# Performance work log

Measured on AMD Instinct MI355X. Metric: run time of the kernel, lower is better.

The kernel has to match this reference:

```python
import jax, jax.numpy as jnp
import numpy as np

B, S, D, H, N = 4, 2048, 512, 8, 64
HD = D // H  # head dim


def setup_inputs() -> dict:
    key = jax.random.key(0)
    ks = jax.random.split(key, 4)
    s = 0.02  # xavier-ish init scale
    return {
        "x": jax.random.normal(ks[0], (B, S, D), jnp.float32),
        "in_proj_w": jax.random.normal(ks[1], (3 * D, D), jnp.float32) * s,
        "in_proj_b": jnp.zeros((3 * D,), jnp.float32),
        "out_proj_w": jax.random.normal(ks[2], (D, D), jnp.float32) * s,
        "out_proj_b": jnp.zeros((D,), jnp.float32),
        "content_w": jax.random.normal(ks[3], (N, D), jnp.float32) * s,
        "content_b": jnp.zeros((N,), jnp.float32),
        "k_input": 16,
    }


def _fwd_core(x, in_proj_w, in_proj_b, out_proj_w, out_proj_b, content_w, content_b):
    # torch nn.MultiheadAttention (batch_first, eval/no dropout), self-attention
    qkv = jnp.einsum("bsd,ed->bse", x, in_proj_w) + in_proj_b  # [B,S,3D]
    q, k, v = jnp.split(qkv, 3, axis=-1)
    to_heads = lambda t: t.reshape(B, S, H, HD).transpose(0, 2, 1, 3)  # [B,H,S,hd]
    q, k, v = to_heads(q), to_heads(k), to_heads(v)
    scores = jnp.einsum("bhqd,bhkd->bhqk", q, k) / jnp.sqrt(jnp.float32(HD))
    attn = jax.nn.softmax(scores, axis=-1)  # [B,H,S,S] (need_weights=True path)
    ctx = jnp.einsum("bhqk,bhkd->bhqd", attn, v)
    ctx = ctx.transpose(0, 2, 1, 3).reshape(B, S, D)
    attended = jnp.einsum("bsd,ed->bse", ctx, out_proj_w) + out_proj_b  # [B,S,D]

    # content_to_neuron
    aff = jnp.einsum("bsd,nd->bsn", attended, content_w) + content_b  # [B,S,N]

    # position importance: mean over heads, sum over keys, normalize
    pos_imp = attn.mean(axis=1).sum(axis=2)  # [B,S]
    pos_imp = pos_imp / (pos_imp.sum(axis=1, keepdims=True) + 1e-8)

    weighted = (aff * pos_imp[..., None]).sum(axis=1)  # [B,N]
    final = 0.5 * weighted + 0.3 * aff.max(axis=1) + 0.2 * aff.mean(axis=1)
    probs = jax.nn.softmax(final, axis=-1)
    return final, probs, attended


def reference(x, in_proj_w, in_proj_b, out_proj_w, out_proj_b, content_w, content_b, k_input):
    final, probs, attended = _fwd_core(
        x, in_proj_w, in_proj_b, out_proj_w, out_proj_b, content_w, content_b
    )
    _, input_idx = jax.lax.top_k(final, k_input)  # [B,k]
    one_hot = jnp.zeros_like(probs).at[jnp.arange(B)[:, None], input_idx].set(1.0)
    # straight-through: value == one_hot, gradient flows through probs
    routing_weights = jax.lax.stop_gradient(one_hot - probs) + probs
    return input_idx, routing_weights, attended
```

## Files before the change

### kernel.cpp

```cpp
#include <hip/hip_runtime.h>
#include <hip/hip_bf16.h>

typedef unsigned short u16;
typedef __bf16 bf16x8 __attribute__((ext_vector_type(8)));
typedef u16 u16x8 __attribute__((ext_vector_type(8)));
typedef u16 u16x4 __attribute__((ext_vector_type(4)));
typedef float f32x4 __attribute__((ext_vector_type(4)));

__device__ __forceinline__ u16 f2bf(float f) {
  union { float f; unsigned u; } v; v.f = f;
  return (u16)((v.u + 0x7FFFu + ((v.u >> 16) & 1u)) >> 16);
}
__device__ __forceinline__ float bf2f(u16 h) {
  union { unsigned u; float f; } v; v.u = ((unsigned)h) << 16;
  return v.f;
}
struct BfPair { u16 hi, lo; };
__device__ __forceinline__ BfPair split2(float f) {
  BfPair r;
  r.hi = f2bf(f);
  r.lo = f2bf(f - bf2f(r.hi));
  return r;
}
__device__ __forceinline__ bf16x8 as_bf16x8(u16x8 u) {
  union { u16x8 u; bf16x8 b; } v; v.u = u; return v.b;
}

#define MFMA16(a, b, c) __builtin_amdgcn_mfma_f32_16x16x32_bf16((a), (b), (c), 0, 0, 0)

#define GLD16(gp, lp)                                                          \
  __builtin_amdgcn_global_load_lds(                                            \
      (const __attribute__((address_space(1))) void*)(gp),                     \
      (__attribute__((address_space(3))) void*)(lp), 16, 0, 0)

__global__ __launch_bounds__(256) void split_kernel(
    const float* __restrict__ src, u16* __restrict__ hi, u16* __restrict__ lo, int n4)
{
  int i = blockIdx.x * 256 + threadIdx.x;
  if (i >= n4) return;
  f32x4 v = ((const f32x4*)src)[i];
  u16x4 h, l;
  #pragma unroll
  for (int j = 0; j < 4; j++) { BfPair p = split2(v[j]); h[j] = p.hi; l[j] = p.lo; }
  ((u16x4*)hi)[i] = h;
  ((u16x4*)lo)[i] = l;
}

template<int OUT_PLANES>
__global__ __launch_bounds__(256, 3) void gemm_nt(
    const u16* __restrict__ Ah, const u16* __restrict__ Al,
    const u16* __restrict__ Bh, const u16* __restrict__ Bl,
    const float* __restrict__ bias,
    void* __restrict__ C0, void* __restrict__ C1,
    int M, int N, int K)
{
  __shared__ u16 Ash[128 * 32], Asl[128 * 32];
  __shared__ u16 Bsh[128 * 32], Bsl[128 * 32];
  const int t = threadIdx.x;
  const int lane = t & 63, w = t >> 6;
  const int l15 = lane & 15, g = lane >> 4;
  const int m0 = blockIdx.x * 128, n0 = blockIdx.y * 128;

  const int lrow = lane >> 2;
  const int lchunk = lane & 3;

  f32x4 acc[4][4] = {};

  for (int k0 = 0; k0 < K; k0 += 32) {
    __syncthreads();
    #pragma unroll
    for (int q = 0; q < 2; q++) {
      const int row = w * 32 + q * 16 + lrow;
      const int sw = lchunk ^ (row & 3) ^ ((row >> 2) & 3);
      const size_t ga = (size_t)(m0 + row) * K + k0 + sw * 8;
      const size_t gb = (size_t)(n0 + row) * K + k0 + sw * 8;
      const int ldsbase = (w * 32 + q * 16) * 32;
      GLD16(Ah + ga, &Ash[ldsbase]);
      GLD16(Al + ga, &Asl[ldsbase]);
      GLD16(Bh + gb, &Bsh[ldsbase]);
      GLD16(Bl + gb, &Bsl[ldsbase]);
    }
    __syncthreads();

    bf16x8 bh[4], bl[4];
    #pragma unroll
    for (int n = 0; n < 4; n++) {
      const int row = (w & 1) * 64 + n * 16 + l15;
      const int slot = g ^ (row & 3) ^ ((row >> 2) & 3);
      const int idx = row * 32 + slot * 8;
      bh[n] = *(const bf16x8*)&Bsh[idx];
      bl[n] = *(const bf16x8*)&Bsl[idx];
    }
    #pragma unroll
    for (int m = 0; m < 4; m++) {
      const int row = (w >> 1) * 64 + m * 16 + l15;
      const int slot = g ^ (row & 3) ^ ((row >> 2) & 3);
      const int idx = row * 32 + slot * 8;
      bf16x8 ah = *(const bf16x8*)&Ash[idx];
      bf16x8 al = *(const bf16x8*)&Asl[idx];
      #pragma unroll
      for (int n = 0; n < 4; n++) {
        acc[m][n] = MFMA16(ah, bh[n], acc[m][n]);
        acc[m][n] = MFMA16(ah, bl[n], acc[m][n]);
        acc[m][n] = MFMA16(al, bh[n], acc[m][n]);
      }
    }
  }

  const int r0 = m0 + (w >> 1) * 64;
  const int c0 = n0 + (w & 1) * 64;
  float bs[4];
  #pragma unroll
  for (int n = 0; n < 4; n++) bs[n] = bias[c0 + n * 16 + l15];
  #pragma unroll
  for (int m = 0; m < 4; m++)
    #pragma unroll
    for (int n = 0; n < 4; n++) {
      const int col = c0 + n * 16 + l15;
      #pragma unroll
      for (int r = 0; r < 4; r++) {
        float v = acc[m][n][r] + bs[n];
        size_t idx = (size_t)(r0 + m * 16 + g * 4 + r) * N + col;
        if (OUT_PLANES) {
          BfPair pp = split2(v);
          ((u16*)C0)[idx] = pp.hi;
          ((u16*)C1)[idx] = pp.lo;
        } else {
          ((float*)C0)[idx] = v;
        }
      }
    }
}

__global__ __launch_bounds__(256, 2) void attn_kernel(
    const u16* __restrict__ qkv_h, const u16* __restrict__ qkv_l,
    u16* __restrict__ ctx_h, u16* __restrict__ ctx_l)
{
  const int bh = blockIdx.x;
  const int b = bh >> 3, h = bh & 7;
  const int q0 = blockIdx.y * 128;
  const int t = threadIdx.x, lane = t & 63, w = t >> 6;
  const int l15 = lane & 15, g = lane >> 4;

  __shared__ u16 Ksh[64 * 72], Ksl[64 * 72];
  __shared__ u16 Vsh[64 * 72], Vsl[64 * 72];
  __shared__ u16 Psh[4][32 * 72], Psl[4][32 * 72];

  const size_t rowbase = (size_t)b * 2048;

  bf16x8 qbh[2][2], qbl[2][2];
  #pragma unroll
  for (int i = 0; i < 2; i++) {
    size_t qoff = (rowbase + q0 + i * 64 + w * 16 + l15) * 1536 + h * 64 + g * 8;
    #pragma unroll
    for (int kc = 0; kc < 2; kc++) {
      u16x8 uh = *(const u16x8*)(qkv_h + qoff + kc * 32);
      u16x8 ul = *(const u16x8*)(qkv_l + qoff + kc * 32);
      #pragma unroll
      for (int j = 0; j < 8; j++) {
        uh[j] = f2bf(bf2f(uh[j]) * 0.125f);
        ul[j] = f2bf(bf2f(ul[j]) * 0.125f);
      }
      qbh[i][kc] = as_bf16x8(uh);
      qbl[i][kc] = as_bf16x8(ul);
    }
  }

  f32x4 oacc[2][4] = {};
  float l_q[2] = {0.f, 0.f};

  u16x8 skh[2], skl[2], svh[2], svl[2];
  #pragma unroll
  for (int rep = 0; rep < 2; rep++) {
    int c = t + rep * 256;
    int row = c >> 3, col = (c & 7) * 8;
    size_t off = (rowbase + row) * 1536 + h * 64 + col;
    skh[rep] = *(const u16x8*)(qkv_h + off + 512);
    skl[rep] = *(const u16x8*)(qkv_l + off + 512);
    svh[rep] = *(const u16x8*)(qkv_h + off + 1024);
    svl[rep] = *(const u16x8*)(qkv_l + off + 1024);
  }

  for (int kt = 0; kt < 32; kt++) {
    __syncthreads();
    #pragma unroll
    for (int rep = 0; rep < 2; rep++) {
      int c = t + rep * 256;
      int row = c >> 3, col = (c & 7) * 8;
      *(u16x8*)&Ksh[row * 72 + col] = skh[rep];
      *(u16x8*)&Ksl[row * 72 + col] = skl[rep];
      int rk = (row + col) & 63;
      #pragma unroll
      for (int j = 0; j < 8; j++) {
        Vsh[(col + j) * 72 + rk] = svh[rep][j];
        Vsl[(col + j) * 72 + rk] = svl[rep][j];
      }
    }
    if (kt + 1 < 32) {
      #pragma unroll
      for (int rep = 0; rep < 2; rep++) {
        int c = t + rep * 256;
        int row = c >> 3, col = (c & 7) * 8;
        size_t off = (rowbase + (kt + 1) * 64 + row) * 1536 + h * 64 + col;
        skh[rep] = *(const u16x8*)(qkv_h + off + 512);
        skl[rep] = *(const u16x8*)(qkv_l + off + 512);
        svh[rep] = *(const u16x8*)(qkv_h + off + 1024);
        svl[rep] = *(const u16x8*)(qkv_l + off + 1024);
      }
    }
    __syncthreads();

    f32x4 sa0[4] = {}, sa1[4] = {};
    #pragma unroll
    for (int kc = 0; kc < 2; kc++) {
      #pragma unroll
      for (int cb = 0; cb < 4; cb++) {
        int ki = (cb * 16 + l15) * 72 + g * 8 + kc * 32;
        bf16x8 kh = *(const bf16x8*)&Ksh[ki];
        bf16x8 kl = *(const bf16x8*)&Ksl[ki];
        sa0[cb] = MFMA16(kh, qbh[0][kc], sa0[cb]);
        sa1[cb] = MFMA16(kh, qbh[1][kc], sa1[cb]);
        sa0[cb] = MFMA16(kh, qbl[0][kc], sa0[cb]);
        sa1[cb] = MFMA16(kh, qbl[1][kc], sa1[cb]);
        sa0[cb] = MFMA16(kl, qbh[0][kc], sa0[cb]);
        sa1[cb] = MFMA16(kl, qbh[1][kc], sa1[cb]);
      }
    }

    #pragma unroll
    for (int i = 0; i < 2; i++) {
      f32x4* sa = (i == 0) ? sa0 : sa1;
      float rs = 0.f;
      #pragma unroll
      for (int cb = 0; cb < 4; cb++)
        #pragma unroll
        for (int r = 0; r < 4; r++) {
          float p = __expf(sa[cb][r]);
          sa[cb][r] = p;
          rs += p;
        }
      rs += __shfl_xor(rs, 16, 64);
      rs += __shfl_xor(rs, 32, 64);
      l_q[i] += rs;

      #pragma unroll
      for (int cb = 0; cb < 4; cb++) {
        u16x4 ph, pl;
        #pragma unroll
        for (int r = 0; r < 4; r++) {
          BfPair pp = split2(sa[cb][r]);
          ph[r] = pp.hi; pl[r] = pp.lo;
        }
        int pi = (i * 16 + l15) * 72 + cb * 16 + g * 4;
        *(u16x4*)&Psh[w][pi] = ph;
        *(u16x4*)&Psl[w][pi] = pl;
      }
    }

    asm volatile("s_waitcnt lgkmcnt(0)" ::: "memory");
    __builtin_amdgcn_sched_barrier(0);

    bf16x8 pah[2][2], pal[2][2];
    #pragma unroll
    for (int i = 0; i < 2; i++)
      #pragma unroll
      for (int kc = 0; kc < 2; kc++) {
        int pb = (i * 16 + l15) * 72 + kc * 32 + g * 8;
        pah[i][kc] = *(const bf16x8*)&Psh[w][pb];
        pal[i][kc] = *(const bf16x8*)&Psl[w][pb];
      }

    #pragma unroll
    for (int kc = 0; kc < 2; kc++) {
      #pragma unroll
      for (int cb = 0; cb < 4; cb++) {
        int d = cb * 16 + l15;
        int rk0 = (g * 8 + kc * 32 + (d & 56)) & 63;
        bf16x8 vbh = *(const bf16x8*)&Vsh[d * 72 + rk0];
        bf16x8 vbl = *(const bf16x8*)&Vsl[d * 72 + rk0];
        oacc[0][cb] = MFMA16(pah[0][kc], vbh, oacc[0][cb]);
        oacc[1][cb] = MFMA16(pah[1][kc], vbh, oacc[1][cb]);
        oacc[0][cb] = MFMA16(pah[0][kc], vbl, oacc[0][cb]);
        oacc[1][cb] = MFMA16(pah[1][kc], vbl, oacc[1][cb]);
        oacc[0][cb] = MFMA16(pal[0][kc], vbh, oacc[0][cb]);
        oacc[1][cb] = MFMA16(pal[1][kc], vbh, oacc[1][cb]);
      }
    }
  }

  #pragma unroll
  for (int i = 0; i < 2; i++)
    #pragma unroll
    for (int r = 0; r < 4; r++) {
      float lq = __shfl(l_q[i], g * 4 + r, 64);
      float inv = 1.0f / lq;
      int row = q0 + i * 64 + w * 16 + g * 4 + r;
      size_t base = (rowbase + row) * 512 + h * 64;
      #pragma unroll
      for (int cb = 0; cb < 4; cb++) {
        BfPair pp = split2(oacc[i][cb][r] * inv);
        ctx_h[base + cb * 16 + l15] = pp.hi;
        ctx_l[base + cb * 16 + l15] = pp.lo;
      }
    }
}

__global__ __launch_bounds__(256) void aff_reduce(
    const float* __restrict__ att, const float* __restrict__ cw,
    const float* __restrict__ cbias, float* __restrict__ psum, float* __restrict__ pmax)
{
  const int b = blockIdx.x, sb = blockIdx.y;
  const int t = threadIdx.x;
  const int n = t & 63, rg = t >> 6;
  __shared__ float cws[64 * 65];
  __shared__ float ats[32 * 65];
  __shared__ float reds[256], redm[256];

  float acc[8] = {};
  for (int kc = 0; kc < 8; kc++) {
    __syncthreads();
    #pragma unroll
    for (int i = 0; i < 4; i++) {
      int c = t + i * 256;
      int row = c >> 4, col = (c & 15) * 4;
      f32x4 v = *(const f32x4*)(cw + (size_t)row * 512 + kc * 64 + col);
      cws[row * 65 + col + 0] = v[0]; cws[row * 65 + col + 1] = v[1];
      cws[row * 65 + col + 2] = v[2]; cws[row * 65 + col + 3] = v[3];
    }
    #pragma unroll
    for (int i = 0; i < 2; i++) {
      int c = t + i * 256;
      int row = c >> 4, col = (c & 15) * 4;
      f32x4 v = *(const f32x4*)(att + ((size_t)b * 2048 + sb * 32 + row) * 512 + kc * 64 + col);
      ats[row * 65 + col + 0] = v[0]; ats[row * 65 + col + 1] = v[1];
      ats[row * 65 + col + 2] = v[2]; ats[row * 65 + col + 3] = v[3];
    }
    __syncthreads();
    for (int k = 0; k < 64; k++) {
      float c = cws[n * 65 + k];
      #pragma unroll
      for (int r = 0; r < 8; r++)
        acc[r] += ats[(rg * 8 + r) * 65 + k] * c;
    }
  }
  const float bn = cbias[n];
  float s = 0.f, m = -1e30f;
  #pragma unroll
  for (int r = 0; r < 8; r++) {
    float v = acc[r] + bn;
    s += v; m = fmaxf(m, v);
  }
  reds[t] = s; redm[t] = m;
  __syncthreads();
  if (t < 64) {
    float ss = reds[t] + reds[64 + t] + reds[128 + t] + reds[192 + t];
    float mm = fmaxf(fmaxf(redm[t], redm[64 + t]), fmaxf(redm[128 + t], redm[192 + t]));
    psum[((size_t)b * 64 + sb) * 64 + t] = ss;
    pmax[((size_t)b * 64 + sb) * 64 + t] = mm;
  }
}

__global__ void final_topk(const float* __restrict__ psum, const float* __restrict__ pmax,
                           float* __restrict__ out)
{
  __shared__ float fin[4][64];
  const int t = threadIdx.x;
  const int b = t >> 6, n = t & 63;
  float s = 0.f, m = -1e30f;
  for (int j = 0; j < 64; j++) {
    s += psum[((size_t)b * 64 + j) * 64 + n];
    m = fmaxf(m, pmax[((size_t)b * 64 + j) * 64 + n]);
  }
  const float mean = s * (1.0f / 2048.0f);
  fin[b][n] = 0.5f * mean + 0.3f * m + 0.2f * mean;
  __syncthreads();
  if (t < 4) {
    unsigned long long chosen = 0ull;
    for (int j = 0; j < 16; j++) {
      float best = -3e38f; int bi = 0;
      for (int nn = 0; nn < 64; nn++) {
        float v = fin[t][nn];
        if (!((chosen >> nn) & 1ull) && v > best) { best = v; bi = nn; }
      }
      chosen |= 1ull << bi;
      out[t * 16 + j] = (float)bi;
    }
    for (int nn = 0; nn < 64; nn++)
      out[64 + t * 64 + nn] = ((chosen >> nn) & 1ull) ? 1.0f : 0.0f;
  }
}

extern "C" void kernel_launch(void* const* d_in, const int* in_sizes, int n_in,
                              void* d_out, int out_size, void* d_ws, size_t ws_size,
                              hipStream_t stream) {
  const float* x    = (const float*)d_in[0];
  const float* win  = (const float*)d_in[1];
  const float* bin  = (const float*)d_in[2];
  const float* wout = (const float*)d_in[3];
  const float* bout = (const float*)d_in[4];
  const float* cw   = (const float*)d_in[5];
  const float* cbv  = (const float*)d_in[6];
  (void)in_sizes; (void)n_in; (void)ws_size; (void)out_size;

  float* out = (float*)d_out;
  char* ws = (char*)d_ws;
  u16*   qkv_h = (u16*)ws;
  u16*   qkv_l = (u16*)(ws + 25165824);
  u16*   ctx_h = (u16*)(ws + 50331648);
  u16*   ctx_l = (u16*)(ws + 58720256);
  float* psum  = (float*)(ws + 67108864);
  float* pmax  = (float*)(ws + 67174400);
  u16*   winh  = (u16*)(ws + 67239936);
  u16*   winl  = (u16*)(ws + 68812800);
  u16*   wouth = (u16*)(ws + 70385664);
  u16*   woutl = (u16*)(ws + 70909952);
  u16*   xh = ctx_h, *xl = ctx_l;
  float* attended = out + 320;

  split_kernel<<<4096, 256, 0, stream>>>(x, xh, xl, 1048576);
  split_kernel<<<768, 256, 0, stream>>>(win, winh, winl, 196608);
  split_kernel<<<256, 256, 0, stream>>>(wout, wouth, woutl, 65536);

  gemm_nt<1><<<dim3(64, 12), 256, 0, stream>>>(
      xh, xl, winh, winl, bin, qkv_h, qkv_l, 8192, 1536, 512);
  attn_kernel<<<dim3(32, 16), 256, 0, stream>>>(qkv_h, qkv_l, ctx_h, ctx_l);
  gemm_nt<0><<<dim3(64, 4), 256, 0, stream>>>(
      ctx_h, ctx_l, wouth, woutl, bout, attended, nullptr, 8192, 512, 512);
  aff_reduce<<<dim3(4, 64), 256, 0, stream>>>(attended, cw, cbv, psum, pmax);
  final_topk<<<1, 256, 0, stream>>>(psum, pmax, out);
}
```

Baseline: 283.6 us.

## Enlarge attention blocks, single P buffer, and fold out_proj into content projection

```diff
diff --git a/kernel.cpp b/kernel.cpp
--- a/kernel.cpp
+++ b/kernel.cpp
@@ -2,6 +2,7 @@
 #include <hip/hip_bf16.h>
 
 typedef unsigned short u16;
+typedef unsigned int u32;
 typedef __bf16 bf16x8 __attribute__((ext_vector_type(8)));
 typedef u16 u16x8 __attribute__((ext_vector_type(8)));
 typedef u16 u16x4 __attribute__((ext_vector_type(4)));
@@ -14,6 +15,9 @@
 __device__ __forceinline__ float bf2f(u16 h) {
   union { unsigned u; float f; } v; v.u = ((unsigned)h) << 16;
   return v.f;
+}
+__device__ __forceinline__ float asf(u32 u) {
+  union { unsigned u; float f; } v; v.u = u; return v.f;
 }
 struct BfPair { u16 hi, lo; };
 __device__ __forceinline__ BfPair split2(float f) {
@@ -24,6 +28,11 @@
 }
 __device__ __forceinline__ bf16x8 as_bf16x8(u16x8 u) {
   union { u16x8 u; bf16x8 b; } v; v.u = u; return v.b;
+}
+__device__ __forceinline__ u32 cvt_pk(float a, float b) {
+  u32 r;
+  asm volatile("v_cvt_pk_bf16_f32 %0, %1, %2" : "=v"(r) : "v"(a), "v"(b));
+  return r;
 }
 
 #define MFMA16(a, b, c) __builtin_amdgcn_mfma_f32_16x16x32_bf16((a), (b), (c), 0, 0, 0)
@@ -60,7 +69,6 @@
   const int lane = t & 63, w = t >> 6;
   const int l15 = lane & 15, g = lane >> 4;
   const int m0 = blockIdx.x * 128, n0 = blockIdx.y * 128;
-
   const int lrow = lane >> 2;
   const int lchunk = lane & 3;
 
@@ -132,34 +140,37 @@
     }
 }
 
-__global__ __launch_bounds__(256, 2) void attn_kernel(
+__global__ __launch_bounds__(512, 2) void attn_kernel(
     const u16* __restrict__ qkv_h, const u16* __restrict__ qkv_l,
     u16* __restrict__ ctx_h, u16* __restrict__ ctx_l)
 {
   const int bh = blockIdx.x;
   const int b = bh >> 3, h = bh & 7;
-  const int q0 = blockIdx.y * 128;
+  const int q0 = blockIdx.y * 256;
   const int t = threadIdx.x, lane = t & 63, w = t >> 6;
   const int l15 = lane & 15, g = lane >> 4;
+  const int wh = w >> 2, wl = w & 3;
 
   __shared__ u16 Ksh[64 * 72], Ksl[64 * 72];
   __shared__ u16 Vsh[64 * 72], Vsl[64 * 72];
-  __shared__ u16 Psh[4][32 * 72], Psl[4][32 * 72];
+  __shared__ u16 Ps[8][32 * 72];
 
   const size_t rowbase = (size_t)b * 2048;
+  const float QSC = 0.125f * 1.44269504088896f;
 
   bf16x8 qbh[2][2], qbl[2][2];
   #pragma unroll
   for (int i = 0; i < 2; i++) {
-    size_t qoff = (rowbase + q0 + i * 64 + w * 16 + l15) * 1536 + h * 64 + g * 8;
+    size_t qoff = (rowbase + q0 + wh * 128 + i * 64 + wl * 16 + l15) * 1536 + h * 64 + g * 8;
     #pragma unroll
     for (int kc = 0; kc < 2; kc++) {
       u16x8 uh = *(const u16x8*)(qkv_h + qoff + kc * 32);
       u16x8 ul = *(const u16x8*)(qkv_l + qoff + kc * 32);
       #pragma unroll
       for (int j = 0; j < 8; j++) {
-        uh[j] = f2bf(bf2f(uh[j]) * 0.125f);
-        ul[j] = f2bf(bf2f(ul[j]) * 0.125f);
+        float v = (bf2f(uh[j]) + bf2f(ul[j])) * QSC;
+        BfPair p = split2(v);
+        uh[j] = p.hi; ul[j] = p.lo;
       }
       qbh[i][kc] = as_bf16x8(uh);
       qbl[i][kc] = as_bf16x8(ul);
@@ -169,44 +180,34 @@
   f32x4 oacc[2][4] = {};
   float l_q[2] = {0.f, 0.f};
 
-  u16x8 skh[2], skl[2], svh[2], svl[2];
-  #pragma unroll
-  for (int rep = 0; rep < 2; rep++) {
-    int c = t + rep * 256;
-    int row = c >> 3, col = (c & 7) * 8;
-    size_t off = (rowbase + row) * 1536 + h * 64 + col;
-    skh[rep] = *(const u16x8*)(qkv_h + off + 512);
-    skl[rep] = *(const u16x8*)(qkv_l + off + 512);
-    svh[rep] = *(const u16x8*)(qkv_h + off + 1024);
-    svl[rep] = *(const u16x8*)(qkv_l + off + 1024);
+  const int srow = t >> 3, scol = (t & 7) * 8;
+  u16x8 skh, skl, svh, svl;
+  {
+    size_t off = (rowbase + srow) * 1536 + h * 64 + scol;
+    skh = *(const u16x8*)(qkv_h + off + 512);
+    skl = *(const u16x8*)(qkv_l + off + 512);
+    svh = *(const u16x8*)(qkv_h + off + 1024);
+    svl = *(const u16x8*)(qkv_l + off + 1024);
   }
 
   for (int kt = 0; kt < 32; kt++) {
     __syncthreads();
-    #pragma unroll
-    for (int rep = 0; rep < 2; rep++) {
-      int c = t + rep * 256;
-      int row = c >> 3, col = (c & 7) * 8;
-      *(u16x8*)&Ksh[row * 72 + col] = skh[rep];
-      *(u16x8*)&Ksl[row * 72 + col] = skl[rep];
-      int rk = (row + col) & 63;
+    {
+      *(u16x8*)&Ksh[srow * 72 + scol] = skh;
+      *(u16x8*)&Ksl[srow * 72 + scol] = skl;
+      int rk = (srow + scol) & 63;
       #pragma unroll
       for (int j = 0; j < 8; j++) {
-        Vsh[(col + j) * 72 + rk] = svh[rep][j];
-        Vsl[(col + j) * 72 + rk] = svl[rep][j];
+        Vsh[(scol + j) * 72 + rk] = svh[j];
+        Vsl[(scol + j) * 72 + rk] = svl[j];
       }
     }
     if (kt + 1 < 32) {
-      #pragma unroll
-      for (int rep = 0; rep < 2; rep++) {
-        int c = t + rep * 256;
-        int row = c >> 3, col = (c & 7) * 8;
-        size_t off = (rowbase + (kt + 1) * 64 + row) * 1536 + h * 64 + col;
-        skh[rep] = *(const u16x8*)(qkv_h + off + 512);
-        skl[rep] = *(const u16x8*)(qkv_l + off + 512);
-        svh[rep] = *(const u16x8*)(qkv_h + off + 1024);
-        svl[rep] = *(const u16x8*)(qkv_l + off + 1024);
-      }
+      size_t off = (rowbase + (kt + 1) * 64 + srow) * 1536 + h * 64 + scol;
+      skh = *(const u16x8*)(qkv_h + off + 512);
+      skl = *(const u16x8*)(qkv_l + off + 512);
+      svh = *(const u16x8*)(qkv_h + off + 1024);
+      svl = *(const u16x8*)(qkv_l + off + 1024);
     }
     __syncthreads();
 
@@ -227,48 +228,64 @@
       }
     }
 
+    u32 hw[2][4][2], lw[2][4][2];
     #pragma unroll
     for (int i = 0; i < 2; i++) {
       f32x4* sa = (i == 0) ? sa0 : sa1;
       float rs = 0.f;
       #pragma unroll
-      for (int cb = 0; cb < 4; cb++)
+      for (int cb = 0; cb < 4; cb++) {
         #pragma unroll
         for (int r = 0; r < 4; r++) {
-          float p = __expf(sa[cb][r]);
+          float p = exp2f(sa[cb][r]);
           sa[cb][r] = p;
           rs += p;
         }
+        u32 h0 = cvt_pk(sa[cb][0], sa[cb][1]);
+        u32 h1 = cvt_pk(sa[cb][2], sa[cb][3]);
+        hw[i][cb][0] = h0; hw[i][cb][1] = h1;
+        float l0 = sa[cb][0] - asf(h0 << 16);
+        float l1 = sa[cb][1] - asf(h0 & 0xFFFF0000u);
+        float l2 = sa[cb][2] - asf(h1 << 16);
+        float l3 = sa[cb][3] - asf(h1 & 0xFFFF0000u);
+        lw[i][cb][0] = cvt_pk(l0, l1);
+        lw[i][cb][1] = cvt_pk(l2, l3);
+      }
       rs += __shfl_xor(rs, 16, 64);
       rs += __shfl_xor(rs, 32, 64);
       l_q[i] += rs;
-
+    }
+
+    #pragma unroll
+    for (int i = 0; i < 2; i++)
       #pragma unroll
       for (int cb = 0; cb < 4; cb++) {
-        u16x4 ph, pl;
-        #pragma unroll
-        for (int r = 0; r < 4; r++) {
-          BfPair pp = split2(sa[cb][r]);
-          ph[r] = pp.hi; pl[r] = pp.lo;
-        }
-        int pi = (i * 16 + l15) * 72 + cb * 16 + g * 4;
-        *(u16x4*)&Psh[w][pi] = ph;
-        *(u16x4*)&Psl[w][pi] = pl;
-      }
-    }
-
+        u32* dst = (u32*)&Ps[w][(i * 16 + l15) * 72 + cb * 16 + g * 4];
+        dst[0] = hw[i][cb][0]; dst[1] = hw[i][cb][1];
+      }
     asm volatile("s_waitcnt lgkmcnt(0)" ::: "memory");
     __builtin_amdgcn_sched_barrier(0);
-
     bf16x8 pah[2][2], pal[2][2];
     #pragma unroll
     for (int i = 0; i < 2; i++)
       #pragma unroll
-      for (int kc = 0; kc < 2; kc++) {
-        int pb = (i * 16 + l15) * 72 + kc * 32 + g * 8;
-        pah[i][kc] = *(const bf16x8*)&Psh[w][pb];
-        pal[i][kc] = *(const bf16x8*)&Psl[w][pb];
-      }
+      for (int kc = 0; kc < 2; kc++)
+        pah[i][kc] = *(const bf16x8*)&Ps[w][(i * 16 + l15) * 72 + kc * 32 + g * 8];
+    __builtin_amdgcn_sched_barrier(0);
+    #pragma unroll
+    for (int i = 0; i < 2; i++)
+      #pragma unroll
+      for (int cb = 0; cb < 4; cb++) {
+        u32* dst = (u32*)&Ps[w][(i * 16 + l15) * 72 + cb * 16 + g * 4];
+        dst[0] = lw[i][cb][0]; dst[1] = lw[i][cb][1];
+      }
+    asm volatile("s_waitcnt lgkmcnt(0)" ::: "memory");
+    __builtin_amdgcn_sched_barrier(0);
+    #pragma unroll
+    for (int i = 0; i < 2; i++)
+      #pragma unroll
+      for (int kc = 0; kc < 2; kc++)
+        pal[i][kc] = *(const bf16x8*)&Ps[w][(i * 16 + l15) * 72 + kc * 32 + g * 8];
 
     #pragma unroll
     for (int kc = 0; kc < 2; kc++) {
@@ -294,7 +311,7 @@
     for (int r = 0; r < 4; r++) {
       float lq = __shfl(l_q[i], g * 4 + r, 64);
       float inv = 1.0f / lq;
-      int row = q0 + i * 64 + w * 16 + g * 4 + r;
+      int row = q0 + wh * 128 + i * 64 + wl * 16 + g * 4 + r;
       size_t base = (rowbase + row) * 512 + h * 64;
       #pragma unroll
       for (int cb = 0; cb < 4; cb++) {
@@ -305,74 +322,159 @@
     }
 }
 
-__global__ __launch_bounds__(256) void aff_reduce(
-    const float* __restrict__ att, const float* __restrict__ cw,
-    const float* __restrict__ cbias, float* __restrict__ psum, float* __restrict__ pmax)
+__global__ __launch_bounds__(256) void compute_m(
+    const float* __restrict__ cw, const float* __restrict__ wout,
+    const float* __restrict__ bout, const float* __restrict__ cbias,
+    u16* __restrict__ mh, u16* __restrict__ ml, float* __restrict__ cb2)
 {
-  const int b = blockIdx.x, sb = blockIdx.y;
+  __shared__ float wouts[64][68];
+  __shared__ float cws[64][65];
   const int t = threadIdx.x;
-  const int n = t & 63, rg = t >> 6;
-  __shared__ float cws[64 * 65];
-  __shared__ float ats[32 * 65];
-  __shared__ float reds[256], redm[256];
-
-  float acc[8] = {};
-  for (int kc = 0; kc < 8; kc++) {
+  const int n = t & 63, dg = t >> 6;
+  const int d0 = blockIdx.x * 64;
+  float acc[16] = {};
+
+  for (int e0 = 0; e0 < 512; e0 += 64) {
     __syncthreads();
     #pragma unroll
     for (int i = 0; i < 4; i++) {
       int c = t + i * 256;
-      int row = c >> 4, col = (c & 15) * 4;
-      f32x4 v = *(const f32x4*)(cw + (size_t)row * 512 + kc * 64 + col);
-      cws[row * 65 + col + 0] = v[0]; cws[row * 65 + col + 1] = v[1];
-      cws[row * 65 + col + 2] = v[2]; cws[row * 65 + col + 3] = v[3];
-    }
-    #pragma unroll
-    for (int i = 0; i < 2; i++) {
-      int c = t + i * 256;
-      int row = c >> 4, col = (c & 15) * 4;
-      f32x4 v = *(const f32x4*)(att + ((size_t)b * 2048 + sb * 32 + row) * 512 + kc * 64 + col);
-      ats[row * 65 + col + 0] = v[0]; ats[row * 65 + col + 1] = v[1];
-      ats[row * 65 + col + 2] = v[2]; ats[row * 65 + col + 3] = v[3];
-    }
-    __syncthreads();
-    for (int k = 0; k < 64; k++) {
-      float c = cws[n * 65 + k];
-      #pragma unroll
-      for (int r = 0; r < 8; r++)
-        acc[r] += ats[(rg * 8 + r) * 65 + k] * c;
-    }
-  }
-  const float bn = cbias[n];
-  float s = 0.f, m = -1e30f;
-  #pragma unroll
-  for (int r = 0; r < 8; r++) {
-    float v = acc[r] + bn;
-    s += v; m = fmaxf(m, v);
-  }
-  reds[t] = s; redm[t] = m;
+      int row = c >> 4, col4 = (c & 15) * 4;
+      f32x4 wv = *(const f32x4*)(wout + (size_t)(e0 + row) * 512 + d0 + col4);
+      wouts[row][col4 + 0] = wv[0]; wouts[row][col4 + 1] = wv[1];
+      wouts[row][col4 + 2] = wv[2]; wouts[row][col4 + 3] = wv[3];
+      f32x4 cv = *(const f32x4*)(cw + (size_t)row * 512 + e0 + col4);
+      cws[row][col4 + 0] = cv[0]; cws[row][col4 + 1] = cv[1];
+      cws[row][col4 + 2] = cv[2]; cws[row][col4 + 3] = cv[3];
+    }
+    __syncthreads();
+    for (int e = 0; e < 64; e++) {
+      float cv = cws[n][e];
+      #pragma unroll
+      for (int q = 0; q < 4; q++) {
+        f32x4 wv = *(const f32x4*)&wouts[e][dg * 16 + q * 4];
+        acc[q * 4 + 0] += wv[0] * cv; acc[q * 4 + 1] += wv[1] * cv;
+        acc[q * 4 + 2] += wv[2] * cv; acc[q * 4 + 3] += wv[3] * cv;
+      }
+    }
+  }
+  #pragma unroll
+  for (int dd = 0; dd < 16; dd++) {
+    BfPair p = split2(acc[dd]);
+    size_t idx = (size_t)n * 512 + d0 + dg * 16 + dd;
+    mh[idx] = p.hi; ml[idx] = p.lo;
+  }
+  if (blockIdx.x == 0 && t < 64) {
+    float s = cbias[t];
+    for (int e = 0; e < 512; e++) s += cw[(size_t)t * 512 + e] * bout[e];
+    cb2[t] = s;
+  }
+}
+
+__global__ __launch_bounds__(256) void aff_mfma(
+    const u16* __restrict__ ch, const u16* __restrict__ cl,
+    const u16* __restrict__ mh, const u16* __restrict__ ml,
+    float* __restrict__ psum, float* __restrict__ pmax)
+{
+  __shared__ u16 Ash[128 * 32], Asl[128 * 32];
+  __shared__ u16 Bsh[64 * 32], Bsl[64 * 32];
+  __shared__ float redS[4 * 64], redM[4 * 64];
+  const int t = threadIdx.x;
+  const int lane = t & 63, w = t >> 6;
+  const int l15 = lane & 15, g = lane >> 4;
+  const int lrow = lane >> 2, lchunk = lane & 3;
+  const int blk = blockIdx.x;
+  const size_t row0 = (size_t)blk * 128;
+
+  f32x4 acc[2][4] = {};
+
+  for (int k0 = 0; k0 < 512; k0 += 32) {
+    __syncthreads();
+    #pragma unroll
+    for (int q = 0; q < 2; q++) {
+      const int row = w * 32 + q * 16 + lrow;
+      const int sw = lchunk ^ (row & 3) ^ ((row >> 2) & 3);
+      const size_t ga = (row0 + row) * 512 + k0 + sw * 8;
+      const int ldsbase = (w * 32 + q * 16) * 32;
+      GLD16(ch + ga, &Ash[ldsbase]);
+      GLD16(cl + ga, &Asl[ldsbase]);
+    }
+    {
+      const int row = w * 16 + lrow;
+      const int sw = lchunk ^ (row & 3) ^ ((row >> 2) & 3);
+      const size_t gb = (size_t)row * 512 + k0 + sw * 8;
+      GLD16(mh + gb, &Bsh[(w * 16) * 32]);
+      GLD16(ml + gb, &Bsl[(w * 16) * 32]);
+    }
+    __syncthreads();
+
+    bf16x8 bh[4], bl[4];
+    #pragma unroll
+    for (int n = 0; n < 4; n++) {
+      const int row = n * 16 + l15;
+      const int slot = g ^ (row & 3) ^ ((row >> 2) & 3);
+      const int idx = row * 32 + slot * 8;
+      bh[n] = *(const bf16x8*)&Bsh[idx];
+      bl[n] = *(const bf16x8*)&Bsl[idx];
+    }
+    #pragma unroll
+    for (int m = 0; m < 2; m++) {
+      const int row = w * 32 + m * 16 + l15;
+      const int slot = g ^ (row & 3) ^ ((row >> 2) & 3);
+      const int idx = row * 32 + slot * 8;
+      bf16x8 ah = *(const bf16x8*)&Ash[idx];
+      bf16x8 al = *(const bf16x8*)&Asl[idx];
+      #pragma unroll
+      for (int n = 0; n < 4; n++) {
+        acc[m][n] = MFMA16(ah, bh[n], acc[m][n]);
+        acc[m][n] = MFMA16(ah, bl[n], acc[m][n]);
+        acc[m][n] = MFMA16(al, bh[n], acc[m][n]);
+      }
+    }
+  }
+
+  #pragma unroll
+  for (int nf = 0; nf < 4; nf++) {
+    float ts = 0.f, tm = -1e30f;
+    #pragma unroll
+    for (int m = 0; m < 2; m++)
+      #pragma unroll
+      for (int r = 0; r < 4; r++) {
+        float v = acc[m][nf][r];
+        ts += v; tm = fmaxf(tm, v);
+      }
+    ts += __shfl_xor(ts, 16, 64); ts += __shfl_xor(ts, 32, 64);
+    tm = fmaxf(tm, __shfl_xor(tm, 16, 64));
+    tm = fmaxf(tm, __shfl_xor(tm, 32, 64));
+    if (g == 0) {
+      redS[w * 64 + nf * 16 + l15] = ts;
+      redM[w * 64 + nf * 16 + l15] = tm;
+    }
+  }
   __syncthreads();
   if (t < 64) {
-    float ss = reds[t] + reds[64 + t] + reds[128 + t] + reds[192 + t];
-    float mm = fmaxf(fmaxf(redm[t], redm[64 + t]), fmaxf(redm[128 + t], redm[192 + t]));
-    psum[((size_t)b * 64 + sb) * 64 + t] = ss;
-    pmax[((size_t)b * 64 + sb) * 64 + t] = mm;
+    float ss = redS[t] + redS[64 + t] + redS[128 + t] + redS[192 + t];
+    float mm = fmaxf(fmaxf(redM[t], redM[64 + t]), fmaxf(redM[128 + t], redM[192 + t]));
+    psum[(size_t)blk * 64 + t] = ss;
+    pmax[(size_t)blk * 64 + t] = mm;
   }
 }
 
 __global__ void final_topk(const float* __restrict__ psum, const float* __restrict__ pmax,
-                           float* __restrict__ out)
+                           const float* __restrict__ cb2, float* __restrict__ out)
 {
   __shared__ float fin[4][64];
   const int t = threadIdx.x;
   const int b = t >> 6, n = t & 63;
   float s = 0.f, m = -1e30f;
-  for (int j = 0; j < 64; j++) {
-    s += psum[((size_t)b * 64 + j) * 64 + n];
-    m = fmaxf(m, pmax[((size_t)b * 64 + j) * 64 + n]);
-  }
-  const float mean = s * (1.0f / 2048.0f);
-  fin[b][n] = 0.5f * mean + 0.3f * m + 0.2f * mean;
+  for (int j = 0; j < 16; j++) {
+    s += psum[((size_t)b * 16 + j) * 64 + n];
+    m = fmaxf(m, pmax[((size_t)b * 16 + j) * 64 + n]);
+  }
+  const float c2 = cb2[n];
+  const float mean = s * (1.0f / 2048.0f) + c2;
+  const float mx = m + c2;
+  fin[b][n] = 0.7f * mean + 0.3f * mx;
   __syncthreads();
   if (t < 4) {
     unsigned long long chosen = 0ull;
@@ -409,12 +511,15 @@
   u16*   ctx_h = (u16*)(ws + 50331648);
   u16*   ctx_l = (u16*)(ws + 58720256);
   float* psum  = (float*)(ws + 67108864);
-  float* pmax  = (float*)(ws + 67174400);
+  float* pmax  = (float*)(ws + 67125248);
+  float* cb2   = (float*)(ws + 67141632);
   u16*   winh  = (u16*)(ws + 67239936);
   u16*   winl  = (u16*)(ws + 68812800);
   u16*   wouth = (u16*)(ws + 70385664);
   u16*   woutl = (u16*)(ws + 70909952);
   u16*   xh = ctx_h, *xl = ctx_l;
+  u16*   mh = qkv_h;
+  u16*   ml = qkv_h + 32768;
   float* attended = out + 320;
 
   split_kernel<<<4096, 256, 0, stream>>>(x, xh, xl, 1048576);
@@ -423,9 +528,10 @@
 
   gemm_nt<1><<<dim3(64, 12), 256, 0, stream>>>(
       xh, xl, winh, winl, bin, qkv_h, qkv_l, 8192, 1536, 512);
-  attn_kernel<<<dim3(32, 16), 256, 0, stream>>>(qkv_h, qkv_l, ctx_h, ctx_l);
+  attn_kernel<<<dim3(32, 8), 512, 0, stream>>>(qkv_h, qkv_l, ctx_h, ctx_l);
   gemm_nt<0><<<dim3(64, 4), 256, 0, stream>>>(
       ctx_h, ctx_l, wouth, woutl, bout, attended, nullptr, 8192, 512, 512);
-  aff_reduce<<<dim3(4, 64), 256, 0, stream>>>(attended, cw, cbv, psum, pmax);
-  final_topk<<<1, 256, 0, stream>>>(psum, pmax, out);
-}
+  compute_m<<<8, 256, 0, stream>>>(cw, wout, bout, cbv, mh, ml, cb2);
+  aff_mfma<<<64, 256, 0, stream>>>(ctx_h, ctx_l, mh, ml, psum, pmax);
+  final_topk<<<1, 256, 0, stream>>>(psum, pmax, cb2, out);
+}
```

Result: slower. 303.2 us (+6.9%).
